# Performance work log

Measured on AMD Instinct MI355X. Metric: run time of the kernel, lower is better.

Reference implementation:

```python
import jax, jax.numpy as jnp
import numpy as np

C = 512
GROUPS = 16
EPS = 1e-6


def group_norm(x, gamma, beta):
    # x: (b, c, h, w)
    b, c, h, w = x.shape
    xg = x.reshape(b, GROUPS, c // GROUPS, h, w)
    mean = xg.mean(axis=(2, 3, 4), keepdims=True)
    var = xg.var(axis=(2, 3, 4), keepdims=True)
    xn = ((xg - mean) * jax.lax.rsqrt(var + EPS)).reshape(b, c, h, w)
    return xn * gamma[None, :, None, None] + beta[None, :, None, None]


def setup_inputs() -> dict:
    key = jax.random.key(0)
    ks = jax.random.split(key, 9)
    scale = 1.0 / np.sqrt(C)
    x = jax.random.normal(ks[0], (32, C, 32, 32), dtype=jnp.float32)
    return {
        "x": x,
        "gn_gamma": jnp.ones((C,), jnp.float32),
        "gn_beta": jnp.zeros((C,), jnp.float32),
        "wq": jax.random.normal(ks[1], (C, C), jnp.float32) * scale,
        "bq": jnp.zeros((C,), jnp.float32),
        "wk": jax.random.normal(ks[2], (C, C), jnp.float32) * scale,
        "bk": jnp.zeros((C,), jnp.float32),
        "wv": jax.random.normal(ks[3], (C, C), jnp.float32) * scale,
        "bv": jnp.zeros((C,), jnp.float32),
        "wp": jax.random.normal(ks[4], (C, C), jnp.float32) * scale,
        "bp": jnp.zeros((C,), jnp.float32),
    }


def reference(x, gn_gamma, gn_beta, wq, bq, wk, bk, wv, bv, wp, bp):
    b, c, h, w = x.shape
    hn = group_norm(x, gn_gamma, gn_beta).reshape(b, c, h * w)  # (b, c, n)
    # 1x1 convs == per-token channel GEMMs
    q = jnp.einsum('oc,bcn->bon', wq, hn) + bq[None, :, None]
    k = jnp.einsum('oc,bcn->bon', wk, hn) + bk[None, :, None]
    v = jnp.einsum('oc,bcn->bon', wv, hn) + bv[None, :, None]
    # scores: (b, n, m) = q^T k, scaled
    s = jnp.einsum('bcn,bcm->bnm', q, k) * (float(c) ** -0.5)
    # original subtracts the global max (shift-invariant) then softmax over dim 2
    s = s - jnp.max(s)
    attn = jax.nn.softmax(s, axis=2)
    # h_ = v @ attn^T  -> (b, c, n)
    out = jnp.einsum('bcm,bnm->bcn', v, attn)
    out = jnp.einsum('oc,bcn->bon', wp, out) + bp[None, :, None]
    return x + out.reshape(b, c, h, w)
```

## Files before the change

kernel.cpp:

```cpp
#include <hip/hip_runtime.h>
#include <hip/hip_bf16.h>

typedef unsigned short u16;
typedef __attribute__((ext_vector_type(8))) short bf16x8;
typedef __attribute__((ext_vector_type(4))) float f32x4;

#define FENCE asm volatile("" ::: "memory")
#define BARRIER() do { FENCE; __builtin_amdgcn_s_barrier(); FENCE; } while (0)
#define LGKM0 asm volatile("s_waitcnt lgkmcnt(0)" ::: "memory")

__device__ __forceinline__ u16 f2bf(float f) {
  union { float f; unsigned u; } a; a.f = f;
  unsigned r = a.u + 0x7fffu + ((a.u >> 16) & 1u);
  return (u16)(r >> 16);
}

__device__ __forceinline__ u16 f2h(float f) {
  union { _Float16 h; u16 u; } c; c.h = (_Float16)f; return c.u;
}

__device__ __forceinline__ void stage_ht(const u16* __restrict__ g, int ldg,
                                         u16* __restrict__ s, int tid) {
  int lane = tid & 63, wave = tid >> 6;
#pragma unroll
  for (int t = 0; t < 2; ++t) {
    int cbase = t * 512 + wave * 64;
    int c = cbase + lane;
    int row = c >> 3;
    int q = (c & 7) ^ (row & 7);
    __builtin_amdgcn_global_load_lds(
        (const __attribute__((address_space(1))) unsigned int*)(g + (long)row * ldg + (q << 3)),
        (__attribute__((address_space(3))) unsigned int*)(s + cbase * 8),
        16, 0, 0);
  }
}

__device__ __forceinline__ void ld_a(const u16* __restrict__ Ah, int mh,
                                     int lrow, int quad, int sw, bf16x8 (&a)[4][2]) {
#pragma unroll
  for (int i = 0; i < 4; ++i) {
    int rb = (mh * 64 + i * 16 + lrow) * 64;
#pragma unroll
    for (int ks = 0; ks < 2; ++ks)
      a[i][ks] = *(const bf16x8*)&Ah[rb + (((ks * 4 + quad) ^ sw) << 3)];
  }
}

__device__ __forceinline__ void ld_b(const u16* __restrict__ Bh, int wn1, int nh,
                                     int lrow, int quad, int sw, bf16x8 (&bq)[2][2]) {
#pragma unroll
  for (int j = 0; j < 2; ++j) {
    int rb = (wn1 * 64 + (nh * 2 + j) * 16 + lrow) * 64;
#pragma unroll
    for (int ks = 0; ks < 2; ++ks)
      bq[j][ks] = *(const bf16x8*)&Bh[rb + (((ks * 4 + quad) ^ sw) << 3)];
  }
}

template <int MH, int NH>
__device__ __forceinline__ void mfma_q(bf16x8 (&a)[4][2], bf16x8 (&bq)[2][2],
                                       f32x4 (&acc)[8][4]) {
#pragma unroll
  for (int i = 0; i < 4; ++i)
#pragma unroll
    for (int j = 0; j < 2; ++j) {
      f32x4 c = acc[MH * 4 + i][NH * 2 + j];
      c = __builtin_amdgcn_mfma_f32_16x16x32_bf16(a[i][0], bq[j][0], c, 0, 0, 0);
      c = __builtin_amdgcn_mfma_f32_16x16x32_bf16(a[i][1], bq[j][1], c, 0, 0, 0);
      acc[MH * 4 + i][NH * 2 + j] = c;
    }
}

__device__ __forceinline__ void gemm256_core(
    const u16* __restrict__ Ab, const u16* __restrict__ Bb,
    int lda, int ldb, int K, int tid,
    u16* __restrict__ As, u16* __restrict__ Bs, f32x4 (&acc)[8][4]) {
  int wave = tid >> 6, lane = tid & 63;
  int wm = wave >> 2, wn = wave & 3, wn1 = wn & 1;
  int lrow = lane & 15, quad = lane >> 4;
  int sw = lrow & 7;
#pragma unroll
  for (int i = 0; i < 8; ++i)
#pragma unroll
    for (int j = 0; j < 4; ++j) acc[i][j] = (f32x4){0.f, 0.f, 0.f, 0.f};
  const u16* Ah0 = As + wm * 8192;
  const u16* Ah1 = As + (2 + wm) * 8192;
  const u16* Bh0 = Bs + (wn >> 1) * 8192;
  const u16* Bh1 = Bs + (2 + (wn >> 1)) * 8192;
  int nkt = K >> 6, npair = nkt >> 1;
  stage_ht(Ab, lda, As, tid);
  stage_ht(Ab + 128L * lda, lda, As + 8192, tid);
  stage_ht(Bb, ldb, Bs, tid);
  stage_ht(Bb + 128L * ldb, ldb, Bs + 8192, tid);
  stage_ht(Ab + 64, lda, As + 2 * 8192, tid);
  bf16x8 a[4][2], bq0[2][2], bq1[2][2];
  for (int pr = 0; pr < npair; ++pr) {
    int kt1 = pr * 2 + 1, kt2 = kt1 + 1, kt3 = kt1 + 2;
    bool st2 = kt2 < nkt, st3 = kt3 < nkt;
    asm volatile("s_waitcnt vmcnt(2)" ::: "memory");
    BARRIER();
    ld_a(Ah0, 0, lrow, quad, sw, a);
    ld_b(Bh0, wn1, 0, lrow, quad, sw, bq0);
    stage_ht(Ab + 128L * lda + kt1 * 64, lda, As + 3 * 8192, tid);
    __builtin_amdgcn_s_setprio(1); mfma_q<0, 0>(a, bq0, acc); __builtin_amdgcn_s_setprio(0);
    LGKM0; BARRIER();
    ld_b(Bh0, wn1, 1, lrow, quad, sw, bq1);
    stage_ht(Bb + kt1 * 64, ldb, Bs + 2 * 8192, tid);
    __builtin_amdgcn_s_setprio(1); mfma_q<0, 1>(a, bq1, acc); __builtin_amdgcn_s_setprio(0);
    LGKM0; BARRIER();
    ld_a(Ah0, 1, lrow, quad, sw, a);
    stage_ht(Bb + 128L * ldb + kt1 * 64, ldb, Bs + 3 * 8192, tid);
    __builtin_amdgcn_s_setprio(1); mfma_q<1, 1>(a, bq1, acc); __builtin_amdgcn_s_setprio(0);
    LGKM0; BARRIER();
    if (st2) stage_ht(Ab + kt2 * 64, lda, As, tid);
    __builtin_amdgcn_s_setprio(1); mfma_q<1, 0>(a, bq0, acc); __builtin_amdgcn_s_setprio(0);
    LGKM0;
    if (pr + 1 < npair) asm volatile("s_waitcnt vmcnt(2)" ::: "memory");
    else                asm volatile("s_waitcnt vmcnt(0)" ::: "memory");
    BARRIER();
    ld_a(Ah1, 0, lrow, quad, sw, a);
    ld_b(Bh1, wn1, 0, lrow, quad, sw, bq0);
    if (st2) stage_ht(Ab + 128L * lda + kt2 * 64, lda, As + 8192, tid);
    __builtin_amdgcn_s_setprio(1); mfma_q<0, 0>(a, bq0, acc); __builtin_amdgcn_s_setprio(0);
    LGKM0; BARRIER();
    ld_b(Bh1, wn1, 1, lrow, quad, sw, bq1);
    if (st2) stage_ht(Bb + kt2 * 64, ldb, Bs, tid);
    __builtin_amdgcn_s_setprio(1); mfma_q<0, 1>(a, bq1, acc); __builtin_amdgcn_s_setprio(0);
    LGKM0; BARRIER();
    ld_a(Ah1, 1, lrow, quad, sw, a);
    if (st2) stage_ht(Bb + 128L * ldb + kt2 * 64, ldb, Bs + 8192, tid);
    __builtin_amdgcn_s_setprio(1); mfma_q<1, 1>(a, bq1, acc); __builtin_amdgcn_s_setprio(0);
    LGKM0; BARRIER();
    if (st3) stage_ht(Ab + kt3 * 64, lda, As + 2 * 8192, tid);
    __builtin_amdgcn_s_setprio(1); mfma_q<1, 0>(a, bq0, acc); __builtin_amdgcn_s_setprio(0);
    LGKM0; BARRIER();
  }
}

__device__ __forceinline__ void epi_trans_bf16(
    f32x4 (&acc)[8][4], u16* __restrict__ C, long cbase, int m0, int n0, int ldc,
    const float* __restrict__ bias, float scale, int wm, int wn, int lrow, int quad) {
#pragma unroll
  for (int mf = 0; mf < 8; ++mf) {
    int rowbase = m0 + wm * 128 + mf * 16 + quad * 4;
    float4 b4 = bias ? *(const float4*)&bias[rowbase] : make_float4(0.f, 0.f, 0.f, 0.f);
#pragma unroll
    for (int nf = 0; nf < 4; ++nf) {
      int col = n0 + wn * 64 + nf * 16 + lrow;
      f32x4 a = acc[mf][nf];
      uint2 o;
      o.x = (unsigned)f2bf(a[0] * scale + b4.x) | ((unsigned)f2bf(a[1] * scale + b4.y) << 16);
      o.y = (unsigned)f2bf(a[2] * scale + b4.z) | ((unsigned)f2bf(a[3] * scale + b4.w) << 16);
      *(uint2*)(C + cbase + (long)col * ldc + rowbase) = o;
    }
  }
}

template <int MODE>
__global__ __launch_bounds__(512, 2) void gemm_kernel(
    const u16* __restrict__ Ag, const u16* __restrict__ Bg,
    void* __restrict__ C0, void* __restrict__ C1, void* __restrict__ C2,
    const float* __restrict__ bias0, const float* __restrict__ bias1,
    const float* __restrict__ bias2, const float* __restrict__ resid,
    int lda, int ldb, int ldc,
    long strideA, long strideB, long strideC, int K, float scale) {
  extern __shared__ u16 smem[];
  u16* As = smem;
  u16* Bs = smem + 32768;
  int tid = threadIdx.x;
  int b = blockIdx.z;
  int m0 = blockIdx.y * 256, n0 = blockIdx.x * 256;
  const u16* Ab = Ag + (long)b * strideA + (long)m0 * lda;
  const u16* Bb = Bg + (long)b * strideB + (long)n0 * ldb;
  f32x4 acc[8][4];
  gemm256_core(Ab, Bb, lda, ldb, K, tid, As, Bs, acc);

  int wave = tid >> 6, lane = tid & 63;
  int wm = wave >> 2, wn = wave & 3;
  int lrow = lane & 15, quad = lane >> 4;
  long cbase = (long)b * strideC;

  if (MODE == 0) {
    epi_trans_bf16(acc, (u16*)C0, cbase, m0, n0, ldc, bias0, scale, wm, wn, lrow, quad);
  } else if (MODE == 1) {
#pragma unroll
    for (int mf = 0; mf < 8; ++mf)
#pragma unroll
      for (int r = 0; r < 4; ++r) {
        int row = m0 + wm * 128 + mf * 16 + quad * 4 + r;
#pragma unroll
        for (int nf = 0; nf < 4; ++nf) {
          int col = n0 + wn * 64 + nf * 16 + lrow;
          ((u16*)C0)[cbase + (long)row * ldc + col] = f2h(acc[mf][nf][r] * scale);
        }
      }
  } else if (MODE == 2) {
#pragma unroll
    for (int mf = 0; mf < 8; ++mf)
#pragma unroll
      for (int r = 0; r < 4; ++r) {
        int row = m0 + wm * 128 + mf * 16 + quad * 4 + r;
        float bv = bias0[row];
#pragma unroll
        for (int nf = 0; nf < 4; ++nf) {
          int col = n0 + wn * 64 + nf * 16 + lrow;
          long idx = cbase + (long)row * ldc + col;
          ((float*)C0)[idx] = acc[mf][nf][r] * scale + bv + resid[idx];
        }
      }
  } else {
    int seg = m0 >> 9;
    int ml = m0 & 511;
    if (seg == 0) {
      epi_trans_bf16(acc, (u16*)C0, cbase, ml, n0, 512, bias0, 1.f, wm, wn, lrow, quad);
    } else if (seg == 1) {
      epi_trans_bf16(acc, (u16*)C1, cbase, ml, n0, 512, bias1, 1.f, wm, wn, lrow, quad);
    } else {
#pragma unroll
      for (int mf = 0; mf < 8; ++mf)
#pragma unroll
        for (int r = 0; r < 4; ++r) {
          int row = ml + wm * 128 + mf * 16 + quad * 4 + r;
          float bv = bias2[row];
#pragma unroll
          for (int nf = 0; nf < 4; ++nf) {
            int col = n0 + wn * 64 + nf * 16 + lrow;
            ((u16*)C2)[cbase + (long)row * 1024 + col] = f2bf(acc[mf][nf][r] + bv);
          }
        }
    }
  }
}

__global__ __launch_bounds__(256) void groupnorm_kernel(
    const float* __restrict__ x, const float* __restrict__ gamma,
    const float* __restrict__ beta, u16* __restrict__ hnT) {
  int g = blockIdx.x, b = blockIdx.y;
  const float* xb = x + ((long)b * 512 + g * 32) * 1024;
  int tid = threadIdx.x;
  float s = 0.f, sq = 0.f;
  float4 vals[32];
#pragma unroll
  for (int j = 0; j < 32; ++j) {
    float4 v = *(const float4*)(xb + (long)j * 1024 + tid * 4);
    vals[j] = v;
    s += v.x + v.y + v.z + v.w;
    sq += v.x * v.x + v.y * v.y + v.z * v.z + v.w * v.w;
  }
#pragma unroll
  for (int off = 1; off < 64; off <<= 1) {
    s += __shfl_xor(s, off);
    sq += __shfl_xor(sq, off);
  }
  __shared__ float ls[4], lq[4];
  if ((tid & 63) == 0) { ls[tid >> 6] = s; lq[tid >> 6] = sq; }
  __syncthreads();
  float ts = ls[0] + ls[1] + ls[2] + ls[3];
  float tq = lq[0] + lq[1] + lq[2] + lq[3];
  float mean = ts * (1.f / 32768.f);
  float var = tq * (1.f / 32768.f) - mean * mean;
  float rstd = rsqrtf(var + 1e-6f);
  u16* hb = hnT + (long)b * (1024 * 512) + g * 32;
#pragma unroll
  for (int t = 0; t < 4; ++t) {
    u16 row[32];
#pragma unroll
    for (int j = 0; j < 32; ++j) {
      float xv = ((const float*)&vals[j])[t];
      row[j] = f2bf((xv - mean) * rstd * gamma[g * 32 + j] + beta[g * 32 + j]);
    }
    uint4* dst = (uint4*)(hb + (long)(tid * 4 + t) * 512);
    const uint4* src = (const uint4*)row;
    dst[0] = src[0]; dst[1] = src[1]; dst[2] = src[2]; dst[3] = src[3];
  }
}

__global__ __launch_bounds__(256) void softmax_kernel(u16* __restrict__ s) {
  long row = blockIdx.x;
  u16* sr = s + row * 1024;
  int tid = threadIdx.x;
  union { uint2 u; _Float16 h[4]; } c;
  c.u = *(const uint2*)(sr + tid * 4);
  float v0 = (float)c.h[0], v1 = (float)c.h[1], v2 = (float)c.h[2], v3 = (float)c.h[3];
  float m = fmaxf(fmaxf(v0, v1), fmaxf(v2, v3));
#pragma unroll
  for (int off = 1; off < 64; off <<= 1) m = fmaxf(m, __shfl_xor(m, off));
  __shared__ float lm[4], lsum[4];
  if ((tid & 63) == 0) lm[tid >> 6] = m;
  __syncthreads();
  float rowmax = fmaxf(fmaxf(lm[0], lm[1]), fmaxf(lm[2], lm[3]));
  float e0 = expf(v0 - rowmax), e1 = expf(v1 - rowmax);
  float e2 = expf(v2 - rowmax), e3 = expf(v3 - rowmax);
  float sum = e0 + e1 + e2 + e3;
#pragma unroll
  for (int off = 1; off < 64; off <<= 1) sum += __shfl_xor(sum, off);
  if ((tid & 63) == 0) lsum[tid >> 6] = sum;
  __syncthreads();
  float inv = 1.f / (lsum[0] + lsum[1] + lsum[2] + lsum[3]);
  uint2 o;
  o.x = (unsigned)f2bf(e0 * inv) | ((unsigned)f2bf(e1 * inv) << 16);
  o.y = (unsigned)f2bf(e2 * inv) | ((unsigned)f2bf(e3 * inv) << 16);
  *(uint2*)(sr + tid * 4) = o;
}

__global__ __launch_bounds__(256) void convertw_kernel(
    const float* __restrict__ w0, const float* __restrict__ w1,
    const float* __restrict__ w2, const float* __restrict__ w3,
    u16* __restrict__ out) {
  int wsel = blockIdx.x >> 8;
  const float* src = wsel == 0 ? w0 : wsel == 1 ? w1 : wsel == 2 ? w2 : w3;
  int idx = ((blockIdx.x & 255) * 256 + threadIdx.x) * 4;
  float4 v = *(const float4*)(src + idx);
  uint2 o;
  o.x = (unsigned)f2bf(v.x) | ((unsigned)f2bf(v.y) << 16);
  o.y = (unsigned)f2bf(v.z) | ((unsigned)f2bf(v.w) << 16);
  *(uint2*)(out + (long)wsel * 262144 + idx) = o;
}

extern "C" void kernel_launch(void* const* d_in, const int* in_sizes, int n_in,
                              void* d_out, int out_size, void* d_ws, size_t ws_size,
                              hipStream_t stream) {
  const float* x     = (const float*)d_in[0];
  const float* gamma = (const float*)d_in[1];
  const float* beta  = (const float*)d_in[2];
  const float* wq    = (const float*)d_in[3];
  const float* bq    = (const float*)d_in[4];
  const float* wk    = (const float*)d_in[5];
  const float* bk    = (const float*)d_in[6];
  const float* wv    = (const float*)d_in[7];
  const float* bv    = (const float*)d_in[8];
  const float* wp    = (const float*)d_in[9];
  const float* bp    = (const float*)d_in[10];
  float* out = (float*)d_out;
  char* ws = (char*)d_ws;

  static int attr_done = 0;
  if (!attr_done) {
    hipFuncSetAttribute((const void*)gemm_kernel<0>, hipFuncAttributeMaxDynamicSharedMemorySize, 131072);
    hipFuncSetAttribute((const void*)gemm_kernel<1>, hipFuncAttributeMaxDynamicSharedMemorySize, 131072);
    hipFuncSetAttribute((const void*)gemm_kernel<2>, hipFuncAttributeMaxDynamicSharedMemorySize, 131072);
    hipFuncSetAttribute((const void*)gemm_kernel<3>, hipFuncAttributeMaxDynamicSharedMemorySize, 131072);
    attr_done = 1;
  }

  u16* wbf = (u16*)ws;
  u16* hnT = (u16*)(ws + (2L << 20));
  u16* qT  = (u16*)(ws + (34L << 20));
  u16* kT  = (u16*)(ws + (66L << 20));
  u16* v   = (u16*)(ws + (98L << 20));
  u16* s16 = (u16*)(ws + (130L << 20));
  u16* aoT = hnT;

  const long SB = 512L * 1024;
  const long SS = 1024L * 1024;
  const float scale = 0.044194173824159216f;

  convertw_kernel<<<1024, 256, 0, stream>>>(wq, wk, wv, wp, wbf);
  groupnorm_kernel<<<dim3(16, 32), 256, 0, stream>>>(x, gamma, beta, hnT);

  gemm_kernel<3><<<dim3(4, 6, 32), 512, 131072, stream>>>(
      wbf, hnT, qT, kT, v, bq, bk, bv, nullptr,
      512, 512, 0, 0, SB, SB, 512, 1.f);

  gemm_kernel<1><<<dim3(4, 4, 32), 512, 131072, stream>>>(
      qT, kT, s16, nullptr, nullptr, nullptr, nullptr, nullptr, nullptr,
      512, 512, 1024, SB, SB, SS, 512, scale);

  softmax_kernel<<<32 * 1024, 256, 0, stream>>>(s16);

  gemm_kernel<0><<<dim3(4, 2, 32), 512, 131072, stream>>>(
      v, s16, aoT, nullptr, nullptr, nullptr, nullptr, nullptr, nullptr,
      1024, 1024, 512, SB, SS, SB, 1024, 1.f);

  gemm_kernel<2><<<dim3(4, 2, 32), 512, 131072, stream>>>(
      wbf + 3 * 262144, aoT, out, nullptr, nullptr, bp, nullptr, nullptr, x,
      512, 512, 1024, 0, SB, SB, 512, 1.f);
}
```

Before: 369.3 us.

## Replace phased ping-pong GEMM pipeline with simple double-buffered k-loop

Replaces the hand-scheduled 8-phase main loop of the 256x256 GEMM core with a plain double-buffered loop. The old loop interleaved half-tile LDS staging with MFMA quarters, using explicit vmcnt/lgkmcnt waits and many barriers. Each iteration now takes one __syncthreads, loads all A/B fragments for the current buffer, issues the whole next k-tile's global-to-LDS staging, then runs all MFMAs under raised priority. This removes most barriers and the custom wait logic. In exchange it loses the fine-grained overlap of memory staging with compute and relies on the compiler's waitcnt placement.

```diff
diff --git a/kernel.cpp b/kernel.cpp
--- a/kernel.cpp
+++ b/kernel.cpp
@@ -4,10 +4,6 @@
 typedef unsigned short u16;
 typedef __attribute__((ext_vector_type(8))) short bf16x8;
 typedef __attribute__((ext_vector_type(4))) float f32x4;
-
-#define FENCE asm volatile("" ::: "memory")
-#define BARRIER() do { FENCE; __builtin_amdgcn_s_barrier(); FENCE; } while (0)
-#define LGKM0 asm volatile("s_waitcnt lgkmcnt(0)" ::: "memory")
 
 __device__ __forceinline__ u16 f2bf(float f) {
   union { float f; unsigned u; } a; a.f = f;
@@ -83,57 +79,34 @@
   for (int i = 0; i < 8; ++i)
 #pragma unroll
     for (int j = 0; j < 4; ++j) acc[i][j] = (f32x4){0.f, 0.f, 0.f, 0.f};
-  const u16* Ah0 = As + wm * 8192;
-  const u16* Ah1 = As + (2 + wm) * 8192;
-  const u16* Bh0 = Bs + (wn >> 1) * 8192;
-  const u16* Bh1 = Bs + (2 + (wn >> 1)) * 8192;
-  int nkt = K >> 6, npair = nkt >> 1;
+  int nkt = K >> 6;
   stage_ht(Ab, lda, As, tid);
   stage_ht(Ab + 128L * lda, lda, As + 8192, tid);
   stage_ht(Bb, ldb, Bs, tid);
   stage_ht(Bb + 128L * ldb, ldb, Bs + 8192, tid);
-  stage_ht(Ab + 64, lda, As + 2 * 8192, tid);
-  bf16x8 a[4][2], bq0[2][2], bq1[2][2];
-  for (int pr = 0; pr < npair; ++pr) {
-    int kt1 = pr * 2 + 1, kt2 = kt1 + 1, kt3 = kt1 + 2;
-    bool st2 = kt2 < nkt, st3 = kt3 < nkt;
-    asm volatile("s_waitcnt vmcnt(2)" ::: "memory");
-    BARRIER();
-    ld_a(Ah0, 0, lrow, quad, sw, a);
-    ld_b(Bh0, wn1, 0, lrow, quad, sw, bq0);
-    stage_ht(Ab + 128L * lda + kt1 * 64, lda, As + 3 * 8192, tid);
-    __builtin_amdgcn_s_setprio(1); mfma_q<0, 0>(a, bq0, acc); __builtin_amdgcn_s_setprio(0);
-    LGKM0; BARRIER();
-    ld_b(Bh0, wn1, 1, lrow, quad, sw, bq1);
-    stage_ht(Bb + kt1 * 64, ldb, Bs + 2 * 8192, tid);
-    __builtin_amdgcn_s_setprio(1); mfma_q<0, 1>(a, bq1, acc); __builtin_amdgcn_s_setprio(0);
-    LGKM0; BARRIER();
-    ld_a(Ah0, 1, lrow, quad, sw, a);
-    stage_ht(Bb + 128L * ldb + kt1 * 64, ldb, Bs + 3 * 8192, tid);
-    __builtin_amdgcn_s_setprio(1); mfma_q<1, 1>(a, bq1, acc); __builtin_amdgcn_s_setprio(0);
-    LGKM0; BARRIER();
-    if (st2) stage_ht(Ab + kt2 * 64, lda, As, tid);
-    __builtin_amdgcn_s_setprio(1); mfma_q<1, 0>(a, bq0, acc); __builtin_amdgcn_s_setprio(0);
-    LGKM0;
-    if (pr + 1 < npair) asm volatile("s_waitcnt vmcnt(2)" ::: "memory");
-    else                asm volatile("s_waitcnt vmcnt(0)" ::: "memory");
-    BARRIER();
-    ld_a(Ah1, 0, lrow, quad, sw, a);
-    ld_b(Bh1, wn1, 0, lrow, quad, sw, bq0);
-    if (st2) stage_ht(Ab + 128L * lda + kt2 * 64, lda, As + 8192, tid);
-    __builtin_amdgcn_s_setprio(1); mfma_q<0, 0>(a, bq0, acc); __builtin_amdgcn_s_setprio(0);
-    LGKM0; BARRIER();
-    ld_b(Bh1, wn1, 1, lrow, quad, sw, bq1);
-    if (st2) stage_ht(Bb + kt2 * 64, ldb, Bs, tid);
-    __builtin_amdgcn_s_setprio(1); mfma_q<0, 1>(a, bq1, acc); __builtin_amdgcn_s_setprio(0);
-    LGKM0; BARRIER();
-    ld_a(Ah1, 1, lrow, quad, sw, a);
-    if (st2) stage_ht(Bb + 128L * ldb + kt2 * 64, ldb, Bs + 8192, tid);
-    __builtin_amdgcn_s_setprio(1); mfma_q<1, 1>(a, bq1, acc); __builtin_amdgcn_s_setprio(0);
-    LGKM0; BARRIER();
-    if (st3) stage_ht(Ab + kt3 * 64, lda, As + 2 * 8192, tid);
-    __builtin_amdgcn_s_setprio(1); mfma_q<1, 0>(a, bq0, acc); __builtin_amdgcn_s_setprio(0);
-    LGKM0; BARRIER();
+  for (int kt = 0; kt < nkt; ++kt) {
+    __syncthreads();
+    const u16* Ah = As + ((kt & 1) * 2 + wm) * 8192;
+    const u16* Bh = Bs + ((kt & 1) * 2 + (wn >> 1)) * 8192;
+    bf16x8 a0[4][2], a1[4][2], bq0[2][2], bq1[2][2];
+    ld_a(Ah, 0, lrow, quad, sw, a0);
+    ld_b(Bh, wn1, 0, lrow, quad, sw, bq0);
+    if (kt + 1 < nkt) {
+      long ko = (long)(kt + 1) * 64;
+      int nb = ((kt & 1) ^ 1) * 2;
+      stage_ht(Ab + ko, lda, As + nb * 8192, tid);
+      stage_ht(Ab + 128L * lda + ko, lda, As + (nb + 1) * 8192, tid);
+      stage_ht(Bb + ko, ldb, Bs + nb * 8192, tid);
+      stage_ht(Bb + 128L * ldb + ko, ldb, Bs + (nb + 1) * 8192, tid);
+    }
+    ld_b(Bh, wn1, 1, lrow, quad, sw, bq1);
+    ld_a(Ah, 1, lrow, quad, sw, a1);
+    __builtin_amdgcn_s_setprio(1);
+    mfma_q<0, 0>(a0, bq0, acc);
+    mfma_q<0, 1>(a0, bq1, acc);
+    mfma_q<1, 1>(a1, bq1, acc);
+    mfma_q<1, 0>(a1, bq0, acc);
+    __builtin_amdgcn_s_setprio(0);
   }
 }
 
```

New measurement: 362.5 us. No clear change (-1.8%).
